# Kernel tuning notes

Hardware: AMD Instinct MI355X
Metric: run time of the kernel (lower is better)

Reference implementation:

```python
import jax, jax.numpy as jnp
import numpy as np

# Problem dims (see shape_source)
B, Q_LEN, KV_LEN = 32, 4, 4096          # sequences, new tokens/seq, kv tokens/seq
H_Q, H_KV, D = 32, 8, 128               # query heads, kv heads, head dim
BLOCK_SIZE = 16
BLOCKS_PER_SEQ = KV_LEN // BLOCK_SIZE   # 256
N_BLOCKS = B * BLOCKS_PER_SEQ           # 8192
N_TOKENS = B * Q_LEN                    # 128


def setup_inputs() -> dict:
    key = jax.random.key(0)
    ks = jax.random.split(key, 5)
    query = jax.random.normal(ks[0], (N_TOKENS, H_Q * D), jnp.float32)
    key_new = jax.random.normal(ks[1], (N_TOKENS, H_KV * D), jnp.float32)
    value_new = jax.random.normal(ks[2], (N_TOKENS, H_KV * D), jnp.float32)
    key_cache = jax.random.normal(ks[3], (N_BLOCKS, BLOCK_SIZE, H_KV, D), jnp.float32)
    value_cache = jax.random.normal(ks[4], (N_BLOCKS, BLOCK_SIZE, H_KV, D), jnp.float32)
    # per-sequence block table: random permutation of physical blocks
    rng = np.random.default_rng(0)
    block_tables = rng.permutation(N_BLOCKS).astype(np.int32).reshape(B, BLOCKS_PER_SEQ)
    # new tokens occupy kv positions [KV_LEN-Q_LEN, KV_LEN) of each sequence
    pos = np.arange(KV_LEN - Q_LEN, KV_LEN)                 # [Q_LEN]
    blk = block_tables[:, pos // BLOCK_SIZE]                 # [B, Q_LEN]
    off = pos % BLOCK_SIZE                                   # [Q_LEN]
    new_cache_slots = (blk * BLOCK_SIZE + off[None, :]).reshape(-1).astype(np.int32)
    return {
        "query": query, "key": key_new, "value": value_new,
        "key_cache": key_cache, "value_cache": value_cache,
        "block_tables": jnp.asarray(block_tables),
        "new_cache_slots": jnp.asarray(new_cache_slots),
    }


def reference(query, key, value, key_cache, value_cache, block_tables, new_cache_slots):
    q = query.reshape(N_TOKENS, H_Q, D)
    k_new = key.reshape(N_TOKENS, H_KV, D)
    v_new = value.reshape(N_TOKENS, H_KV, D)

    # scatter new K/V into the paged cache (slot -> block_id, block_offset)
    blk_ids = new_cache_slots // BLOCK_SIZE
    offs = new_cache_slots % BLOCK_SIZE
    key_cache = key_cache.at[blk_ids, offs].set(k_new)
    value_cache = value_cache.at[blk_ids, offs].set(v_new)

    # gather paged KV per sequence: [B, KV_LEN, H_KV, D]
    k = key_cache[block_tables].reshape(B, KV_LEN, H_KV, D)
    v = value_cache[block_tables].reshape(B, KV_LEN, H_KV, D)

    # GQA: qo head j uses kv head j // group (matches repeat_interleave on kv heads)
    G = H_Q // H_KV
    qg = q.reshape(B, Q_LEN, H_KV, G, D)

    sm_scale = D ** -0.5
    scores = jnp.einsum('bqhgd,bkhd->bhgqk', qg, k) * sm_scale  # [B,H_KV,G,Q,KV]

    # causal mask: k_idx - q_idx > KV_LEN - Q_LEN -> -inf
    ki = jnp.arange(KV_LEN)[None, :]
    qi = jnp.arange(Q_LEN)[:, None]
    mask = (ki - qi) > (KV_LEN - Q_LEN)                         # [Q, KV]
    scores = jnp.where(mask, -jnp.inf, scores)

    probs = jax.nn.softmax(scores, axis=-1)
    o = jnp.einsum('bhgqk,bkhd->bqhgd', probs, v)               # [B,Q,H_KV,G,D]
    return o.reshape(N_TOKENS, H_Q * D)
```

## Files before the change

### kernel.cpp

```cpp
#include <hip/hip_runtime.h>


#define BBATCH 32
#define QL 4
#define KVL 4096
#define HQ 32
#define HKV 8
#define DDIM 128
#define GQ 4
#define BLK 16
#define BPS 256
#define NP 16
#define CHUNK 512
#define NCHUNK 8
#define NT 512
#define PBS 20

struct SMemMain {
    float p[CHUNK * PBS];
    float q[NP * DDIM];
    int   bt[BPS];
    float red[8 * NP];
    float fin[NP];
};
union __align__(16) SMem {
    SMemMain m;
    float o[4 * NP * DDIM];
};

__global__ void scatter_kv(const float* __restrict__ knew,
                           const float* __restrict__ vnew,
                           const int* __restrict__ slots,
                           float* __restrict__ kc, float* __restrict__ vc) {
    const int i = blockIdx.x;
    const int t = threadIdx.x;
    const int slot = slots[i];
    const size_t dst = (size_t)slot * (HKV * DDIM) + t * 4;
    const size_t src = (size_t)i * (HKV * DDIM) + t * 4;
    *(float4*)(kc + dst) = *(const float4*)(knew + src);
    *(float4*)(vc + dst) = *(const float4*)(vnew + src);
}

__global__ void __launch_bounds__(NT, 2)
attn_kernel(const float* __restrict__ query,
            const float* __restrict__ kcache,
            const float* __restrict__ vcache,
            const int* __restrict__ btab,
            float* __restrict__ out) {
    __shared__ SMem sm;
    const int h = blockIdx.x;
    const int b = blockIdx.y;
    const int tid = threadIdx.x;
    const int lane = tid & 63;
    const int wave = tid >> 6;
    const int d4 = tid & 31;

    if (tid < BPS) sm.m.bt[tid] = btab[b * BPS + tid];
    {
        const int pr = tid >> 5;
        const int g = pr >> 2, qi = pr & 3;
        const float sc = 0.088388347648318447f;
        const float4 qv = *(const float4*)(query + (size_t)(b * QL + qi) * (HQ * DDIM)
                                           + (h * GQ + g) * DDIM + d4 * 4);
        float4 qs; qs.x = qv.x * sc; qs.y = qv.y * sc; qs.z = qv.z * sc; qs.w = qv.w * sc;
        *(float4*)&sm.m.q[pr * DDIM + d4 * 4] = qs;
    }
    __syncthreads();

    float m_r[NP], l_r[NP], o_r[NP][4];
#pragma unroll
    for (int i = 0; i < NP; ++i) {
        m_r[i] = -__builtin_inff(); l_r[i] = 0.f;
        o_r[i][0] = 0.f; o_r[i][1] = 0.f; o_r[i][2] = 0.f; o_r[i][3] = 0.f;
    }

    for (int c = 0; c < NCHUNK; ++c) {
        const int p = c * CHUNK + tid;
        const float4* kp = (const float4*)(kcache
            + (((size_t)sm.m.bt[p >> 4] * BLK + (p & 15)) * HKV + h) * DDIM);
        float s[NP];
#pragma unroll
        for (int i = 0; i < NP; ++i) s[i] = 0.f;
#pragma unroll 1
        for (int gqi = 0; gqi < 4; ++gqi) {
            float4 k4[8];
#pragma unroll
            for (int j = 0; j < 8; ++j) k4[j] = kp[gqi * 8 + j];
#pragma unroll
            for (int j = 0; j < 8; ++j) {
                const int dbase = (gqi * 8 + j) * 4;
#pragma unroll
                for (int pr = 0; pr < NP; ++pr) {
                    const float4 q4 = *(const float4*)&sm.m.q[pr * DDIM + dbase];
                    s[pr] = fmaf(k4[j].x, q4.x,
                            fmaf(k4[j].y, q4.y,
                            fmaf(k4[j].z, q4.z,
                            fmaf(k4[j].w, q4.w, s[pr]))));
                }
            }
        }
        const int excess = p - (KVL - QL);
        if (excess > 0) {
#pragma unroll
            for (int pr = 0; pr < NP; ++pr)
                if ((pr & 3) < excess) s[pr] = -__builtin_inff();
        }
        float w16[NP];
#pragma unroll
        for (int i = 0; i < NP; ++i) w16[i] = s[i];
#pragma unroll
        for (int off = 32; off >= 1; off >>= 1)
#pragma unroll
            for (int i = 0; i < NP; ++i)
                w16[i] = fmaxf(w16[i], __shfl_xor(w16[i], off, 64));
        if (lane == 0) {
#pragma unroll
            for (int i = 0; i < NP; ++i) sm.m.red[wave * NP + i] = w16[i];
        }
        __syncthreads();
        if (tid < NP) {
            float v = sm.m.red[tid];
#pragma unroll
            for (int w = 1; w < 8; ++w) v = fmaxf(v, sm.m.red[w * NP + tid]);
            sm.m.fin[tid] = v;
        }
        __syncthreads();
        float alpha[NP];
#pragma unroll
        for (int i = 0; i < NP; ++i) {
            const float M = fmaxf(m_r[i], sm.m.fin[i]);
            alpha[i] = __expf(m_r[i] - M);
            m_r[i] = M;
        }
        float pv[NP];
#pragma unroll
        for (int i = 0; i < NP; ++i) pv[i] = __expf(s[i] - m_r[i]);
        *(float4*)&sm.m.p[tid * PBS + 0]  = make_float4(pv[0], pv[1], pv[2], pv[3]);
        *(float4*)&sm.m.p[tid * PBS + 4]  = make_float4(pv[4], pv[5], pv[6], pv[7]);
        *(float4*)&sm.m.p[tid * PBS + 8]  = make_float4(pv[8], pv[9], pv[10], pv[11]);
        *(float4*)&sm.m.p[tid * PBS + 12] = make_float4(pv[12], pv[13], pv[14], pv[15]);
#pragma unroll
        for (int off = 32; off >= 1; off >>= 1)
#pragma unroll
            for (int i = 0; i < NP; ++i)
                pv[i] += __shfl_xor(pv[i], off, 64);
        if (lane == 0) {
#pragma unroll
            for (int i = 0; i < NP; ++i) sm.m.red[wave * NP + i] = pv[i];
        }
        __syncthreads();
        if (tid < NP) {
            float v = sm.m.red[tid];
#pragma unroll
            for (int w = 1; w < 8; ++w) v += sm.m.red[w * NP + tid];
            sm.m.fin[tid] = v;
        }
        __syncthreads();
#pragma unroll
        for (int i = 0; i < NP; ++i) l_r[i] = l_r[i] * alpha[i] + sm.m.fin[i];

#pragma unroll
        for (int i = 0; i < NP; ++i) {
            o_r[i][0] *= alpha[i]; o_r[i][1] *= alpha[i];
            o_r[i][2] *= alpha[i]; o_r[i][3] *= alpha[i];
        }
        const int tg = tid >> 5;
#pragma unroll 1
        for (int jo = 0; jo < 4; ++jo) {
            float4 v4[8]; const float* pp[8];
#pragma unroll
            for (int j = 0; j < 8; ++j) {
                const int tl = tg * 32 + jo * 8 + j;
                const int pa = c * CHUNK + tl;
                const float* vp = vcache
                    + (((size_t)sm.m.bt[pa >> 4] * BLK + (pa & 15)) * HKV + h) * DDIM;
                v4[j] = *(const float4*)(vp + d4 * 4);
                pp[j] = &sm.m.p[tl * PBS];
            }
#pragma unroll
            for (int j = 0; j < 8; ++j) {
                const float4 p0 = *(const float4*)(pp[j] + 0);
                const float4 p1 = *(const float4*)(pp[j] + 4);
                const float4 p2 = *(const float4*)(pp[j] + 8);
                const float4 p3 = *(const float4*)(pp[j] + 12);
                const float pj[NP] = { p0.x, p0.y, p0.z, p0.w, p1.x, p1.y, p1.z, p1.w,
                                       p2.x, p2.y, p2.z, p2.w, p3.x, p3.y, p3.z, p3.w };
#pragma unroll
                for (int i = 0; i < NP; ++i) {
                    o_r[i][0] = fmaf(pj[i], v4[j].x, o_r[i][0]);
                    o_r[i][1] = fmaf(pj[i], v4[j].y, o_r[i][1]);
                    o_r[i][2] = fmaf(pj[i], v4[j].z, o_r[i][2]);
                    o_r[i][3] = fmaf(pj[i], v4[j].w, o_r[i][3]);
                }
            }
        }
    }

    __syncthreads();
#pragma unroll
    for (int i = 0; i < NP; ++i)
#pragma unroll
        for (int j = 0; j < 4; ++j)
            o_r[i][j] += __shfl_xor(o_r[i][j], 32, 64);

    const int slot = wave & 3;
    float* ob = sm.o + slot * (NP * DDIM);
    if (wave < 4 && lane < 32) {
#pragma unroll
        for (int i = 0; i < NP; ++i)
            *(float4*)&ob[i * DDIM + d4 * 4] =
                make_float4(o_r[i][0], o_r[i][1], o_r[i][2], o_r[i][3]);
    }
    __syncthreads();
    if (wave >= 4 && lane < 32) {
#pragma unroll
        for (int i = 0; i < NP; ++i) {
            float4 t = *(float4*)&ob[i * DDIM + d4 * 4];
            t.x += o_r[i][0]; t.y += o_r[i][1]; t.z += o_r[i][2]; t.w += o_r[i][3];
            *(float4*)&ob[i * DDIM + d4 * 4] = t;
        }
    }
    __syncthreads();
    {
        const int pair = tid >> 5;
        const int g = pair >> 2, qi = pair & 3;
        float4 acc = make_float4(0.f, 0.f, 0.f, 0.f);
#pragma unroll
        for (int w2 = 0; w2 < 4; ++w2) {
            const float4 t = *(const float4*)&sm.o[w2 * NP * DDIM + pair * DDIM + d4 * 4];
            acc.x += t.x; acc.y += t.y; acc.z += t.z; acc.w += t.w;
        }
        const float inv = 1.0f / l_r[pair];
        acc.x *= inv; acc.y *= inv; acc.z *= inv; acc.w *= inv;
        *(float4*)(out + (size_t)(b * QL + qi) * (HQ * DDIM)
                   + (h * GQ + g) * DDIM + d4 * 4) = acc;
    }
}

extern "C" void kernel_launch(void* const* d_in, const int* in_sizes, int n_in,
                              void* d_out, int out_size, void* d_ws, size_t ws_size,
                              hipStream_t stream) {
    (void)in_sizes; (void)n_in; (void)out_size; (void)d_ws; (void)ws_size;
    const float* query = (const float*)d_in[0];
    const float* knew  = (const float*)d_in[1];
    const float* vnew  = (const float*)d_in[2];
    float* kcache      = (float*)d_in[3];
    float* vcache      = (float*)d_in[4];
    const int* btab    = (const int*)d_in[5];
    const int* slots   = (const int*)d_in[6];
    float* out         = (float*)d_out;

    scatter_kv<<<dim3(BBATCH * QL), dim3(256), 0, stream>>>(knew, vnew, slots, kcache, vcache);
    attn_kernel<<<dim3(HKV, BBATCH), dim3(NT), 0, stream>>>(query, kcache, vcache, btab, out);
}
```

Before: 1.105 ms.

## Split KV sequence across blocks with flash-decoding partials and combine kernel

Splits each sequence's KV range into four independent workgroups that write partial outputs plus per-row max and sum to workspace, then merges them in a new combine kernel. This quadruples the grid from 256 blocks so more CUs are busy. Inside each chunk, the block-wide max and sum reductions with their four barriers are replaced by per-wave running statistics that are merged once at the end. Register tiles are halved and launch bounds raised to allow more occupancy. The cost is an extra launch and a workspace round trip.

```diff
diff --git a/kernel.cpp b/kernel.cpp
--- a/kernel.cpp
+++ b/kernel.cpp
@@ -11,17 +11,19 @@
 #define BLK 16
 #define BPS 256
 #define NP 16
+#define SPLIT 4
+#define TPW 1024
 #define CHUNK 512
-#define NCHUNK 8
+#define NCH 2
 #define NT 512
 #define PBS 20
+#define WSTRIDE 2080
 
 struct SMemMain {
     float p[CHUNK * PBS];
     float q[NP * DDIM];
-    int   bt[BPS];
-    float red[8 * NP];
-    float fin[NP];
+    int   bt[64];
+    float red[8 * 32];
 };
 union __align__(16) SMem {
     SMemMain m;
@@ -41,21 +43,21 @@
     *(float4*)(vc + dst) = *(const float4*)(vnew + src);
 }
 
-__global__ void __launch_bounds__(NT, 2)
-attn_kernel(const float* __restrict__ query,
-            const float* __restrict__ kcache,
-            const float* __restrict__ vcache,
-            const int* __restrict__ btab,
-            float* __restrict__ out) {
+__global__ void __launch_bounds__(NT, 4)
+attn_partial(const float* __restrict__ query,
+             const float* __restrict__ kcache,
+             const float* __restrict__ vcache,
+             const int* __restrict__ btab,
+             float* __restrict__ ws) {
     __shared__ SMem sm;
     const int h = blockIdx.x;
     const int b = blockIdx.y;
+    const int sp = blockIdx.z;
     const int tid = threadIdx.x;
-    const int lane = tid & 63;
     const int wave = tid >> 6;
     const int d4 = tid & 31;
 
-    if (tid < BPS) sm.m.bt[tid] = btab[b * BPS + tid];
+    if (tid < 64) sm.m.bt[tid] = btab[b * BPS + sp * 64 + tid];
     {
         const int pr = tid >> 5;
         const int g = pr >> 2, qi = pr & 3;
@@ -74,21 +76,23 @@
         o_r[i][0] = 0.f; o_r[i][1] = 0.f; o_r[i][2] = 0.f; o_r[i][3] = 0.f;
     }
 
-    for (int c = 0; c < NCHUNK; ++c) {
-        const int p = c * CHUNK + tid;
+#pragma unroll 1
+    for (int c = 0; c < NCH; ++c) {
+        const int pl = c * CHUNK + tid;
+        const int p  = sp * TPW + pl;
         const float4* kp = (const float4*)(kcache
-            + (((size_t)sm.m.bt[p >> 4] * BLK + (p & 15)) * HKV + h) * DDIM);
+            + (((size_t)sm.m.bt[pl >> 4] * BLK + (p & 15)) * HKV + h) * DDIM);
         float s[NP];
 #pragma unroll
         for (int i = 0; i < NP; ++i) s[i] = 0.f;
 #pragma unroll 1
-        for (int gqi = 0; gqi < 4; ++gqi) {
-            float4 k4[8];
-#pragma unroll
-            for (int j = 0; j < 8; ++j) k4[j] = kp[gqi * 8 + j];
-#pragma unroll
-            for (int j = 0; j < 8; ++j) {
-                const int dbase = (gqi * 8 + j) * 4;
+        for (int gqi = 0; gqi < 8; ++gqi) {
+            float4 k4[4];
+#pragma unroll
+            for (int j = 0; j < 4; ++j) k4[j] = kp[gqi * 4 + j];
+#pragma unroll
+            for (int j = 0; j < 4; ++j) {
+                const int dbase = (gqi * 4 + j) * 4;
 #pragma unroll
                 for (int pr = 0; pr < NP; ++pr) {
                     const float4 q4 = *(const float4*)&sm.m.q[pr * DDIM + dbase];
@@ -105,59 +109,30 @@
             for (int pr = 0; pr < NP; ++pr)
                 if ((pr & 3) < excess) s[pr] = -__builtin_inff();
         }
-        float w16[NP];
-#pragma unroll
-        for (int i = 0; i < NP; ++i) w16[i] = s[i];
+        float wm[NP];
+#pragma unroll
+        for (int i = 0; i < NP; ++i) wm[i] = s[i];
 #pragma unroll
         for (int off = 32; off >= 1; off >>= 1)
 #pragma unroll
             for (int i = 0; i < NP; ++i)
-                w16[i] = fmaxf(w16[i], __shfl_xor(w16[i], off, 64));
-        if (lane == 0) {
-#pragma unroll
-            for (int i = 0; i < NP; ++i) sm.m.red[wave * NP + i] = w16[i];
-        }
-        __syncthreads();
-        if (tid < NP) {
-            float v = sm.m.red[tid];
-#pragma unroll
-            for (int w = 1; w < 8; ++w) v = fmaxf(v, sm.m.red[w * NP + tid]);
-            sm.m.fin[tid] = v;
-        }
-        __syncthreads();
+                wm[i] = fmaxf(wm[i], __shfl_xor(wm[i], off, 64));
         float alpha[NP];
 #pragma unroll
         for (int i = 0; i < NP; ++i) {
-            const float M = fmaxf(m_r[i], sm.m.fin[i]);
+            const float M = fmaxf(m_r[i], wm[i]);
             alpha[i] = __expf(m_r[i] - M);
             m_r[i] = M;
         }
         float pv[NP];
 #pragma unroll
         for (int i = 0; i < NP; ++i) pv[i] = __expf(s[i] - m_r[i]);
+#pragma unroll
+        for (int i = 0; i < NP; ++i) l_r[i] = l_r[i] * alpha[i] + pv[i];
         *(float4*)&sm.m.p[tid * PBS + 0]  = make_float4(pv[0], pv[1], pv[2], pv[3]);
         *(float4*)&sm.m.p[tid * PBS + 4]  = make_float4(pv[4], pv[5], pv[6], pv[7]);
         *(float4*)&sm.m.p[tid * PBS + 8]  = make_float4(pv[8], pv[9], pv[10], pv[11]);
         *(float4*)&sm.m.p[tid * PBS + 12] = make_float4(pv[12], pv[13], pv[14], pv[15]);
-#pragma unroll
-        for (int off = 32; off >= 1; off >>= 1)
-#pragma unroll
-            for (int i = 0; i < NP; ++i)
-                pv[i] += __shfl_xor(pv[i], off, 64);
-        if (lane == 0) {
-#pragma unroll
-            for (int i = 0; i < NP; ++i) sm.m.red[wave * NP + i] = pv[i];
-        }
-        __syncthreads();
-        if (tid < NP) {
-            float v = sm.m.red[tid];
-#pragma unroll
-            for (int w = 1; w < 8; ++w) v += sm.m.red[w * NP + tid];
-            sm.m.fin[tid] = v;
-        }
-        __syncthreads();
-#pragma unroll
-        for (int i = 0; i < NP; ++i) l_r[i] = l_r[i] * alpha[i] + sm.m.fin[i];
 
 #pragma unroll
         for (int i = 0; i < NP; ++i) {
@@ -166,23 +141,24 @@
         }
         const int tg = tid >> 5;
 #pragma unroll 1
-        for (int jo = 0; jo < 4; ++jo) {
-            float4 v4[8]; const float* pp[8];
-#pragma unroll
-            for (int j = 0; j < 8; ++j) {
-                const int tl = tg * 32 + jo * 8 + j;
-                const int pa = c * CHUNK + tl;
+        for (int jo = 0; jo < 8; ++jo) {
+            float4 v4[4];
+#pragma unroll
+            for (int j = 0; j < 4; ++j) {
+                const int tl = tg * 32 + jo * 4 + j;
+                const int pa = sp * TPW + c * CHUNK + tl;
                 const float* vp = vcache
-                    + (((size_t)sm.m.bt[pa >> 4] * BLK + (pa & 15)) * HKV + h) * DDIM;
+                    + (((size_t)sm.m.bt[(c * CHUNK + tl) >> 4] * BLK + (pa & 15)) * HKV + h) * DDIM;
                 v4[j] = *(const float4*)(vp + d4 * 4);
-                pp[j] = &sm.m.p[tl * PBS];
             }
 #pragma unroll
-            for (int j = 0; j < 8; ++j) {
-                const float4 p0 = *(const float4*)(pp[j] + 0);
-                const float4 p1 = *(const float4*)(pp[j] + 4);
-                const float4 p2 = *(const float4*)(pp[j] + 8);
-                const float4 p3 = *(const float4*)(pp[j] + 12);
+            for (int j = 0; j < 4; ++j) {
+                const int tl = tg * 32 + jo * 4 + j;
+                const float* pp = &sm.m.p[tl * PBS];
+                const float4 p0 = *(const float4*)(pp + 0);
+                const float4 p1 = *(const float4*)(pp + 4);
+                const float4 p2 = *(const float4*)(pp + 8);
+                const float4 p3 = *(const float4*)(pp + 12);
                 const float pj[NP] = { p0.x, p0.y, p0.z, p0.w, p1.x, p1.y, p1.z, p1.w,
                                        p2.x, p2.y, p2.z, p2.w, p3.x, p3.y, p3.z, p3.w };
 #pragma unroll
@@ -196,13 +172,36 @@
         }
     }
 
-    __syncthreads();
 #pragma unroll
     for (int i = 0; i < NP; ++i)
 #pragma unroll
         for (int j = 0; j < 4; ++j)
             o_r[i][j] += __shfl_xor(o_r[i][j], 32, 64);
-
+#pragma unroll
+    for (int off = 32; off >= 1; off >>= 1)
+#pragma unroll
+        for (int i = 0; i < NP; ++i)
+            l_r[i] += __shfl_xor(l_r[i], off, 64);
+
+    const int lane = tid & 63;
+    if (lane == 0) {
+#pragma unroll
+        for (int i = 0; i < NP; ++i) {
+            sm.m.red[wave * 32 + i]      = m_r[i];
+            sm.m.red[wave * 32 + 16 + i] = l_r[i];
+        }
+    }
+    __syncthreads();
+    float Mg[NP];
+#pragma unroll
+    for (int i = 0; i < NP; ++i) {
+        float M = sm.m.red[i];
+#pragma unroll
+        for (int w = 1; w < 8; ++w) M = fmaxf(M, sm.m.red[w * 32 + i]);
+        Mg[i] = M;
+        const float e = __expf(m_r[i] - M);
+        o_r[i][0] *= e; o_r[i][1] *= e; o_r[i][2] *= e; o_r[i][3] *= e;
+    }
     const int slot = wave & 3;
     float* ob = sm.o + slot * (NP * DDIM);
     if (wave < 4 && lane < 32) {
@@ -223,24 +222,60 @@
     __syncthreads();
     {
         const int pair = tid >> 5;
-        const int g = pair >> 2, qi = pair & 3;
         float4 acc = make_float4(0.f, 0.f, 0.f, 0.f);
 #pragma unroll
         for (int w2 = 0; w2 < 4; ++w2) {
             const float4 t = *(const float4*)&sm.o[w2 * NP * DDIM + pair * DDIM + d4 * 4];
             acc.x += t.x; acc.y += t.y; acc.z += t.z; acc.w += t.w;
         }
-        const float inv = 1.0f / l_r[pair];
-        acc.x *= inv; acc.y *= inv; acc.z *= inv; acc.w *= inv;
-        *(float4*)(out + (size_t)(b * QL + qi) * (HQ * DDIM)
-                   + (h * GQ + g) * DDIM + d4 * 4) = acc;
-    }
+        float L = 0.f;
+#pragma unroll
+        for (int w = 0; w < 8; ++w)
+            L += sm.m.red[w * 32 + 16 + pair] * __expf(sm.m.red[w * 32 + pair] - Mg[pair]);
+        const size_t widx = ((size_t)((b * HKV + h) * SPLIT + sp)) * WSTRIDE;
+        *(float4*)(ws + widx + pair * DDIM + d4 * 4) = acc;
+        if (d4 == 0) {
+            ws[widx + 2048 + pair] = L;
+            ws[widx + 2064 + pair] = Mg[pair];
+        }
+    }
+}
+
+__global__ void combine_kernel(const float* __restrict__ ws, float* __restrict__ out) {
+    const int h = blockIdx.x, b = blockIdx.y;
+    const int tid = threadIdx.x;
+    const int pair = tid >> 5, d4 = tid & 31;
+    const int g = pair >> 2, qi = pair & 3;
+    const size_t base = ((size_t)((b * HKV + h) * SPLIT)) * WSTRIDE;
+    float Ms[SPLIT], Ls[SPLIT]; float4 Os[SPLIT];
+#pragma unroll
+    for (int s = 0; s < SPLIT; ++s) {
+        Ms[s] = ws[base + s * WSTRIDE + 2064 + pair];
+        Ls[s] = ws[base + s * WSTRIDE + 2048 + pair];
+        Os[s] = *(const float4*)(ws + base + s * WSTRIDE + pair * DDIM + d4 * 4);
+    }
+    float Mg = Ms[0];
+#pragma unroll
+    for (int s = 1; s < SPLIT; ++s) Mg = fmaxf(Mg, Ms[s]);
+    float L = 0.f;
+    float4 acc = make_float4(0.f, 0.f, 0.f, 0.f);
+#pragma unroll
+    for (int s = 0; s < SPLIT; ++s) {
+        const float e = __expf(Ms[s] - Mg);
+        L += Ls[s] * e;
+        acc.x = fmaf(e, Os[s].x, acc.x); acc.y = fmaf(e, Os[s].y, acc.y);
+        acc.z = fmaf(e, Os[s].z, acc.z); acc.w = fmaf(e, Os[s].w, acc.w);
+    }
+    const float inv = 1.0f / L;
+    acc.x *= inv; acc.y *= inv; acc.z *= inv; acc.w *= inv;
+    *(float4*)(out + (size_t)(b * QL + qi) * (HQ * DDIM)
+               + (h * GQ + g) * DDIM + d4 * 4) = acc;
 }
 
 extern "C" void kernel_launch(void* const* d_in, const int* in_sizes, int n_in,
                               void* d_out, int out_size, void* d_ws, size_t ws_size,
                               hipStream_t stream) {
-    (void)in_sizes; (void)n_in; (void)out_size; (void)d_ws; (void)ws_size;
+    (void)in_sizes; (void)n_in; (void)out_size; (void)ws_size;
     const float* query = (const float*)d_in[0];
     const float* knew  = (const float*)d_in[1];
     const float* vnew  = (const float*)d_in[2];
@@ -248,8 +283,10 @@
     float* vcache      = (float*)d_in[4];
     const int* btab    = (const int*)d_in[5];
     const int* slots   = (const int*)d_in[6];
+    float* ws          = (float*)d_ws;
     float* out         = (float*)d_out;
 
     scatter_kv<<<dim3(BBATCH * QL), dim3(256), 0, stream>>>(knew, vnew, slots, kcache, vcache);
-    attn_kernel<<<dim3(HKV, BBATCH), dim3(NT), 0, stream>>>(query, kcache, vcache, btab, out);
-}
+    attn_partial<<<dim3(HKV, BBATCH, SPLIT), dim3(NT), 0, stream>>>(query, kcache, vcache, btab, ws);
+    combine_kernel<<<dim3(HKV, BBATCH), dim3(NT), 0, stream>>>(ws, out);
+}
```

Result: slower. 1.305 ms (+18.1%).
